# Performance work log

Measured on AMD Instinct MI355X. Metric: run time of the kernel, lower is better.

## Reference

```python
import jax, jax.numpy as jnp
import numpy as np

NUM_HEADS = 12
EPS = 1e-6

def setup_inputs() -> dict:
    key = jax.random.key(0)
    ks = jax.random.split(key, 7)
    B, N, C = 16, 4096, 384
    hd = C // NUM_HEADS
    s = 0.02
    return {
        "x": jax.random.normal(ks[0], (B, N, C), jnp.float32),
        "qkv_w": jax.random.normal(ks[1], (3 * C, C), jnp.float32) * s,
        "pos_enc": jax.random.normal(ks[2], (1, N, C), jnp.float32) * s,
        "dwc_w": jax.random.normal(ks[3], (hd, 1, 5, 5), jnp.float32) * s,
        "dwc_b": jnp.zeros((hd,), jnp.float32),
        "proj_w": jax.random.normal(ks[4], (C, C), jnp.float32) * s,
        "proj_b": jnp.zeros((C,), jnp.float32),
    }

def reference(x, qkv_w, pos_enc, dwc_w, dwc_b, proj_w, proj_b):
    B, N, C = x.shape
    H = NUM_HEADS
    hd = C // H
    qkv = x @ qkv_w.T  # (B, N, 3C)
    q, k, v = jnp.split(qkv, 3, axis=-1)
    k = k + pos_enc
    q = jax.nn.relu(q)
    k = jax.nn.relu(k)
    # b n (h c) -> (b h) n c
    def to_heads(t):
        return t.reshape(B, N, H, hd).transpose(0, 2, 1, 3).reshape(B * H, N, hd)
    q, k, v = to_heads(q), to_heads(k), to_heads(v)
    q = q.astype(jnp.float32); k = k.astype(jnp.float32); v = v.astype(jnp.float32)
    # normalizer z: (BH, N)
    z = 1.0 / (jnp.einsum('bic,bc->bi', q, k.sum(axis=1)) + EPS)
    # linear-attention branch (i*j*(c+d) > c*d*(i+j) here)
    kv = jnp.einsum('bjc,bjd->bcd', k, v)  # (BH, hd, hd)
    out = jnp.einsum('bic,bcd,bi->bid', q, kv, z)  # (BH, N, hd)
    # depthwise conv branch over v reshaped to spatial map
    w = int(np.sqrt(N))
    fm = v.reshape(B * H, w, w, hd).transpose(0, 3, 1, 2)  # b (w h) c -> b c w h
    fm = jax.lax.conv_general_dilated(
        fm, dwc_w, window_strides=(1, 1), padding=((2, 2), (2, 2)),
        feature_group_count=hd, dimension_numbers=('NCHW', 'OIHW', 'NCHW'))
    fm = fm + dwc_b[None, :, None, None]
    fm = fm.transpose(0, 2, 3, 1).reshape(B * H, N, hd)  # b c w h -> b (w h) c
    out = out + fm
    # (b h) n c -> b n (h c)
    out = out.reshape(B, H, N, hd).transpose(0, 2, 1, 3).reshape(B, N, C)
    return out @ proj_w.T + proj_b
```

## Files before the change

### kernel.cpp

```cpp
#include <hip/hip_runtime.h>
#include <hip/hip_bf16.h>
#include <cstdint>
#include <cstddef>


typedef __bf16 bf16;
typedef __attribute__((ext_vector_type(8))) __bf16 bf16x8;
typedef __attribute__((ext_vector_type(4))) __bf16 bf16x4;
typedef __attribute__((ext_vector_type(4))) float f32x4;
typedef __attribute__((ext_vector_type(16))) float f32x16;

#define NHEADS 12
#define HD 32
#define BATCH 16
#define SEQ 4096
#define CDIM 384
#define BHN (BATCH*NHEADS)
#define KVPARTS 2

__global__ void convert_w(const float* __restrict__ qkvw, const float* __restrict__ projw,
                          bf16* __restrict__ qkvw_b, bf16* __restrict__ projw_b) {
    int i = blockIdx.x * 256 + threadIdx.x;
    int stride = gridDim.x * 256;
    const int nq = 3 * CDIM * CDIM;
    const int np = CDIM * CDIM;
    for (int idx = i; idx < nq; idx += stride) qkvw_b[idx] = (bf16)qkvw[idx];
    for (int idx = i; idx < np; idx += stride) projw_b[idx] = (bf16)projw[idx];
}

__global__ __launch_bounds__(256, 2)
void gemm_qkv(const float* __restrict__ X, const bf16* __restrict__ Wb,
              const float* __restrict__ pos,
              bf16* __restrict__ qh, bf16* __restrict__ kh, bf16* __restrict__ vh) {
    __shared__ bf16 As[128 * 64];
    __shared__ bf16 Bs[128 * 64];
    const int tid  = threadIdx.x;
    const int lane = tid & 63;
    const int wid  = tid >> 6;
    const int m0   = blockIdx.y * 128;
    const int n0   = blockIdx.x * 128;
    const int wm   = (wid & 1) * 64;
    const int wn   = (wid >> 1) * 64;
    const int lr   = lane & 15;
    const int lq   = lane >> 4;

    f32x4 acc[4][4] = {};

    for (int k0 = 0; k0 < CDIM; k0 += 64) {
        #pragma unroll
        for (int it = 0; it < 4; ++it) {
            int cid = tid + it * 256;
            int r = cid >> 3, c = cid & 7;
            const float* srcA = X + (size_t)(m0 + r) * CDIM + k0 + c * 8;
            float4 f0 = *(const float4*)srcA;
            float4 f1 = *(const float4*)(srcA + 4);
            bf16x8 ha;
            ha[0]=(bf16)f0.x; ha[1]=(bf16)f0.y; ha[2]=(bf16)f0.z; ha[3]=(bf16)f0.w;
            ha[4]=(bf16)f1.x; ha[5]=(bf16)f1.y; ha[6]=(bf16)f1.z; ha[7]=(bf16)f1.w;
            *(bf16x8*)&As[r * 64 + ((c ^ (r & 7))) * 8] = ha;
            *(bf16x8*)&Bs[r * 64 + ((c ^ (r & 7))) * 8] =
                *(const bf16x8*)&Wb[(size_t)(n0 + r) * CDIM + k0 + c * 8];
        }
        __syncthreads();
        #pragma unroll
        for (int ks = 0; ks < 2; ++ks) {
            bf16x8 af[4], bfr[4];
            #pragma unroll
            for (int mi = 0; mi < 4; ++mi) {
                int r = wm + mi * 16 + lr;
                af[mi] = *(const bf16x8*)&As[r * 64 + ((ks * 4 + lq) ^ (r & 7)) * 8];
            }
            #pragma unroll
            for (int ni = 0; ni < 4; ++ni) {
                int r = wn + ni * 16 + lr;
                bfr[ni] = *(const bf16x8*)&Bs[r * 64 + ((ks * 4 + lq) ^ (r & 7)) * 8];
            }
            #pragma unroll
            for (int mi = 0; mi < 4; ++mi)
                #pragma unroll
                for (int ni = 0; ni < 4; ++ni)
                    acc[mi][ni] = __builtin_amdgcn_mfma_f32_16x16x32_bf16(
                        af[mi], bfr[ni], acc[mi][ni], 0, 0, 0);
        }
        __syncthreads();
    }

    const int sec = n0 / CDIM;
    #pragma unroll
    for (int mi = 0; mi < 4; ++mi) {
        #pragma unroll
        for (int ni = 0; ni < 4; ++ni) {
            int n = n0 + wn + ni * 16 + lr;
            int c = n - sec * CDIM;
            int hh = c >> 5, d = c & 31;
            #pragma unroll
            for (int r = 0; r < 4; ++r) {
                int m = m0 + wm + mi * 16 + lq * 4 + r;
                int b = m >> 12, i = m & 4095;
                float v = acc[mi][ni][r];
                size_t dst = ((size_t)(b * NHEADS + hh) * SEQ + i) * HD + d;
                if (sec == 0) {
                    qh[dst] = (bf16)fmaxf(v, 0.f);
                } else if (sec == 1) {
                    v += pos[(size_t)i * CDIM + c];
                    kh[dst] = (bf16)fmaxf(v, 0.f);
                } else {
                    vh[dst] = (bf16)v;
                }
            }
        }
    }
}

__global__ __launch_bounds__(256, 2)
void kv_mfma(const bf16* __restrict__ kh, const bf16* __restrict__ vh,
             float* __restrict__ kv_part, float* __restrict__ ksum_part) {
    __shared__ float red[4 * 1024];
    __shared__ float ksred[4 * 32];
    const int tid  = threadIdx.x;
    const int lane = tid & 63;
    const int w    = tid >> 6;
    const int bh   = blockIdx.y;
    const int part = blockIdx.x;
    const int col  = lane & 31;
    const int half = lane >> 5;
    const bf16* kb = kh + (size_t)bh * SEQ * HD;
    const bf16* vb = vh + (size_t)bh * SEQ * HD;
    const int j0 = part * 2048 + w * 512;

    f32x16 acc = {};
    f32x16 aks = {};
    bf16x8 ones;
    #pragma unroll
    for (int j = 0; j < 8; ++j) ones[j] = (bf16)1.0f;

    for (int s = 0; s < 32; ++s) {
        int jb = j0 + s * 16 + half * 8;
        bf16x8 afr, bfr;
        #pragma unroll
        for (int j = 0; j < 8; ++j) {
            afr[j] = kb[(size_t)(jb + j) * HD + col];
            bfr[j] = vb[(size_t)(jb + j) * HD + col];
        }
        acc = __builtin_amdgcn_mfma_f32_32x32x16_bf16(afr, bfr, acc, 0, 0, 0);
        aks = __builtin_amdgcn_mfma_f32_32x32x16_bf16(afr, ones, aks, 0, 0, 0);
    }

    #pragma unroll
    for (int r = 0; r < 16; ++r) {
        int row = (r & 3) + 8 * (r >> 2) + 4 * half;
        red[w * 1024 + row * 32 + col] = acc[r];
        ksred[w * 32 + row] = aks[r];
    }
    __syncthreads();
    {
        int e = tid * 4;
        f32x4 s4 = *(f32x4*)&red[e];
        s4 += *(f32x4*)&red[1024 + e];
        s4 += *(f32x4*)&red[2048 + e];
        s4 += *(f32x4*)&red[3072 + e];
        *(f32x4*)&kv_part[((size_t)bh * KVPARTS + part) * 1024 + e] = s4;
    }
    if (tid < 32) {
        ksum_part[((size_t)bh * KVPARTS + part) * 32 + tid] =
            ksred[tid] + ksred[32 + tid] + ksred[64 + tid] + ksred[96 + tid];
    }
}

__global__ __launch_bounds__(256, 2)
void attn_out(const bf16* __restrict__ qh, const bf16* __restrict__ vh,
              const float* __restrict__ kv_part, const float* __restrict__ ksum_part,
              const float* __restrict__ dwcw, const float* __restrict__ dwcb,
              bf16* __restrict__ outp) {
    __shared__ bf16 vt[12 * 64 * 32];
    __shared__ float kvl[1024];
    __shared__ float ksl[32];
    __shared__ float wl[25 * 32];
    __shared__ float bl[32];
    const int tid = threadIdx.x;
    const int bh  = blockIdx.y;
    const int ys  = blockIdx.x * 8;
    const bf16* vbase = vh + (size_t)bh * SEQ * HD;

    #pragma unroll
    for (int it = 0; it < 12; ++it) {
        int cid = tid + it * 256;
        int vy = cid >> 8;
        int xx = (cid >> 2) & 63;
        int q  = cid & 3;
        int gy = ys + vy - 2;
        bf16x8 val = {};
        if (gy >= 0 && gy < 64)
            val = *(const bf16x8*)&vbase[((size_t)gy * 64 + xx) * HD + q * 8];
        *(bf16x8*)&vt[(vy * 64 + xx) * HD + q * 8] = val;
    }
    {
        const float* kp = kv_part + (size_t)bh * KVPARTS * 1024;
        f32x4 t = *(const f32x4*)&kp[tid * 4];
        t += *(const f32x4*)&kp[1024 + tid * 4];
        *(f32x4*)&kvl[tid * 4] = t;
    }
    if (tid < 32) {
        const float* sp = ksum_part + (size_t)bh * KVPARTS * 32;
        ksl[tid] = sp[tid] + sp[32 + tid];
        #pragma unroll
        for (int tap = 0; tap < 25; ++tap) wl[tap * 32 + tid] = dwcw[tid * 25 + tap];
        bl[tid] = dwcb[tid];
    }
    __syncthreads();

    const int dq = tid & 7, d0 = dq * 4;
    const int ri = tid >> 3;
    const int b = bh / NHEADS, hh = bh % NHEADS;
    const bf16* qbase = qh + (size_t)bh * SEQ * HD;

    for (int it = 0; it < 16; ++it) {
        int pix = ri + it * 32;
        int yy = pix >> 6;
        int x  = pix & 63;
        int tok = (ys + yy) * 64 + x;
        float zden = 1e-6f;
        float dot0 = 0, dot1 = 0, dot2 = 0, dot3 = 0;
        #pragma unroll
        for (int c4 = 0; c4 < 32; c4 += 4) {
            bf16x4 qv = *(const bf16x4*)&qbase[(size_t)tok * HD + c4];
            #pragma unroll
            for (int u = 0; u < 4; ++u) {
                float qf = (float)qv[u];
                int c = c4 + u;
                zden += qf * ksl[c];
                dot0 += qf * kvl[c * 32 + d0];
                dot1 += qf * kvl[c * 32 + d0 + 1];
                dot2 += qf * kvl[c * 32 + d0 + 2];
                dot3 += qf * kvl[c * 32 + d0 + 3];
            }
        }
        float z = 1.f / zden;
        float f0 = bl[d0], f1 = bl[d0 + 1], f2 = bl[d0 + 2], f3 = bl[d0 + 3];
        int vyc = yy + 2;
        #pragma unroll
        for (int dy = -2; dy <= 2; ++dy) {
            #pragma unroll
            for (int dx = -2; dx <= 2; ++dx) {
                int xx = x + dx;
                if (xx < 0 || xx >= 64) continue;
                int tap = (dy + 2) * 5 + (dx + 2);
                bf16x4 vv = *(const bf16x4*)&vt[((vyc + dy) * 64 + xx) * HD + d0];
                const float* wp = &wl[tap * 32 + d0];
                f0 += (float)vv[0] * wp[0];
                f1 += (float)vv[1] * wp[1];
                f2 += (float)vv[2] * wp[2];
                f3 += (float)vv[3] * wp[3];
            }
        }
        bf16x4 ov;
        ov[0] = (bf16)(dot0 * z + f0);
        ov[1] = (bf16)(dot1 * z + f1);
        ov[2] = (bf16)(dot2 * z + f2);
        ov[3] = (bf16)(dot3 * z + f3);
        *(bf16x4*)&outp[((size_t)b * SEQ + tok) * CDIM + hh * HD + d0] = ov;
    }
}

__global__ __launch_bounds__(256, 2)
void gemm_proj(const bf16* __restrict__ A, const bf16* __restrict__ Wb,
               const float* __restrict__ bias, float* __restrict__ out) {
    __shared__ bf16 As[128 * 64];
    __shared__ bf16 Bs[128 * 64];
    const int tid  = threadIdx.x;
    const int lane = tid & 63;
    const int wid  = tid >> 6;
    const int m0   = blockIdx.y * 128;
    const int n0   = blockIdx.x * 128;
    const int wm   = (wid & 1) * 64;
    const int wn   = (wid >> 1) * 64;
    const int lr   = lane & 15;
    const int lq   = lane >> 4;

    f32x4 acc[4][4] = {};

    for (int k0 = 0; k0 < CDIM; k0 += 64) {
        #pragma unroll
        for (int it = 0; it < 4; ++it) {
            int cid = tid + it * 256;
            int r = cid >> 3, c = cid & 7;
            *(bf16x8*)&As[r * 64 + ((c ^ (r & 7))) * 8] =
                *(const bf16x8*)&A[(size_t)(m0 + r) * CDIM + k0 + c * 8];
            *(bf16x8*)&Bs[r * 64 + ((c ^ (r & 7))) * 8] =
                *(const bf16x8*)&Wb[(size_t)(n0 + r) * CDIM + k0 + c * 8];
        }
        __syncthreads();
        #pragma unroll
        for (int ks = 0; ks < 2; ++ks) {
            bf16x8 af[4], bfr[4];
            #pragma unroll
            for (int mi = 0; mi < 4; ++mi) {
                int r = wm + mi * 16 + lr;
                af[mi] = *(const bf16x8*)&As[r * 64 + ((ks * 4 + lq) ^ (r & 7)) * 8];
            }
            #pragma unroll
            for (int ni = 0; ni < 4; ++ni) {
                int r = wn + ni * 16 + lr;
                bfr[ni] = *(const bf16x8*)&Bs[r * 64 + ((ks * 4 + lq) ^ (r & 7)) * 8];
            }
            #pragma unroll
            for (int mi = 0; mi < 4; ++mi)
                #pragma unroll
                for (int ni = 0; ni < 4; ++ni)
                    acc[mi][ni] = __builtin_amdgcn_mfma_f32_16x16x32_bf16(
                        af[mi], bfr[ni], acc[mi][ni], 0, 0, 0);
        }
        __syncthreads();
    }

    #pragma unroll
    for (int mi = 0; mi < 4; ++mi) {
        #pragma unroll
        for (int ni = 0; ni < 4; ++ni) {
            int n = n0 + wn + ni * 16 + lr;
            float bv = bias[n];
            #pragma unroll
            for (int r = 0; r < 4; ++r) {
                int m = m0 + wm + mi * 16 + lq * 4 + r;
                out[(size_t)m * CDIM + n] = acc[mi][ni][r] + bv;
            }
        }
    }
}

extern "C" void kernel_launch(void* const* d_in, const int* in_sizes, int n_in,
                              void* d_out, int out_size, void* d_ws, size_t ws_size,
                              hipStream_t stream) {
    const float* x     = (const float*)d_in[0];
    const float* qkvw  = (const float*)d_in[1];
    const float* pos   = (const float*)d_in[2];
    const float* dwcw  = (const float*)d_in[3];
    const float* dwcb  = (const float*)d_in[4];
    const float* projw = (const float*)d_in[5];
    const float* projb = (const float*)d_in[6];
    float* out = (float*)d_out;

    char* ws = (char*)d_ws;
    size_t off = 0;
    auto alloc = [&](size_t bytes) -> void* {
        void* p = ws + off;
        off += (bytes + 255) & ~(size_t)255;
        return p;
    };
    bf16* qkvw_b = (bf16*)alloc((size_t)3 * CDIM * CDIM * 2);
    bf16* projw_b = (bf16*)alloc((size_t)CDIM * CDIM * 2);
    bf16* qh  = (bf16*)alloc((size_t)BHN * SEQ * HD * 2);
    bf16* khb = (bf16*)alloc((size_t)BHN * SEQ * HD * 2);
    bf16* vh  = (bf16*)alloc((size_t)BHN * SEQ * HD * 2);
    float* kvb   = (float*)alloc((size_t)BHN * KVPARTS * HD * HD * 4);
    float* ksumb = (float*)alloc((size_t)BHN * KVPARTS * HD * 4);

    hipLaunchKernelGGL(convert_w, dim3(512), dim3(256), 0, stream,
                       qkvw, projw, qkvw_b, projw_b);
    hipLaunchKernelGGL(gemm_qkv, dim3(9, 512), dim3(256), 0, stream,
                       x, qkvw_b, pos, qh, khb, vh);
    hipLaunchKernelGGL(kv_mfma, dim3(KVPARTS, BHN), dim3(256), 0, stream,
                       khb, vh, kvb, ksumb);
    bf16* outp = khb;
    hipLaunchKernelGGL(attn_out, dim3(8, BHN), dim3(256), 0, stream,
                       qh, vh, kvb, ksumb, dwcw, dwcb, outp);
    hipLaunchKernelGGL(gemm_proj, dim3(3, 512), dim3(256), 0, stream,
                       outp, projw_b, projb, out);
}
```

Before: 526.4 us.

## Pre-convert X to bf16 and use direct global-to-LDS loads in GEMMs

X is converted to bf16 in a separate vectorized pass, so gemm_qkv no longer converts fp32 tiles inline and re-reads fp32 X once for each of the nine N tiles. Both GEMMs now fill their LDS tiles with global_load_lds DMA, which skips the register round trip and keeps the XOR swizzle by permuting the source columns. Block indices are also remapped with an XCD-aware swizzle over a 1D grid so neighbouring tiles land on the same die's cache. The cost is an extra kernel pass that writes and re-reads a bf16 copy of X.

```diff
diff --git a/kernel.cpp b/kernel.cpp
--- a/kernel.cpp
+++ b/kernel.cpp
@@ -18,18 +18,52 @@
 #define BHN (BATCH*NHEADS)
 #define KVPARTS 2
 
-__global__ void convert_w(const float* __restrict__ qkvw, const float* __restrict__ projw,
-                          bf16* __restrict__ qkvw_b, bf16* __restrict__ projw_b) {
+__device__ __forceinline__ void gl_lds16(const bf16* g, bf16* l) {
+    __builtin_amdgcn_global_load_lds(
+        (const __attribute__((address_space(1))) unsigned int*)g,
+        (__attribute__((address_space(3))) unsigned int*)l, 16, 0, 0);
+}
+
+__global__ void convert_in(const float* __restrict__ X, const float* __restrict__ qkvw,
+                           const float* __restrict__ projw,
+                           bf16* __restrict__ xb, bf16* __restrict__ qkvw_b,
+                           bf16* __restrict__ projw_b) {
     int i = blockIdx.x * 256 + threadIdx.x;
     int stride = gridDim.x * 256;
-    const int nq = 3 * CDIM * CDIM;
-    const int np = CDIM * CDIM;
-    for (int idx = i; idx < nq; idx += stride) qkvw_b[idx] = (bf16)qkvw[idx];
-    for (int idx = i; idx < np; idx += stride) projw_b[idx] = (bf16)projw[idx];
+    const int nx = (65536 * CDIM) / 8;
+    for (int c = i; c < nx; c += stride) {
+        const float* s = X + (size_t)c * 8;
+        float4 f0 = *(const float4*)s;
+        float4 f1 = *(const float4*)(s + 4);
+        bf16x8 h;
+        h[0]=(bf16)f0.x; h[1]=(bf16)f0.y; h[2]=(bf16)f0.z; h[3]=(bf16)f0.w;
+        h[4]=(bf16)f1.x; h[5]=(bf16)f1.y; h[6]=(bf16)f1.z; h[7]=(bf16)f1.w;
+        *(bf16x8*)&xb[(size_t)c * 8] = h;
+    }
+    const int nq = (3 * CDIM * CDIM) / 8;
+    for (int c = i; c < nq; c += stride) {
+        const float* s = qkvw + (size_t)c * 8;
+        float4 f0 = *(const float4*)s;
+        float4 f1 = *(const float4*)(s + 4);
+        bf16x8 h;
+        h[0]=(bf16)f0.x; h[1]=(bf16)f0.y; h[2]=(bf16)f0.z; h[3]=(bf16)f0.w;
+        h[4]=(bf16)f1.x; h[5]=(bf16)f1.y; h[6]=(bf16)f1.z; h[7]=(bf16)f1.w;
+        *(bf16x8*)&qkvw_b[(size_t)c * 8] = h;
+    }
+    const int np = (CDIM * CDIM) / 8;
+    for (int c = i; c < np; c += stride) {
+        const float* s = projw + (size_t)c * 8;
+        float4 f0 = *(const float4*)s;
+        float4 f1 = *(const float4*)(s + 4);
+        bf16x8 h;
+        h[0]=(bf16)f0.x; h[1]=(bf16)f0.y; h[2]=(bf16)f0.z; h[3]=(bf16)f0.w;
+        h[4]=(bf16)f1.x; h[5]=(bf16)f1.y; h[6]=(bf16)f1.z; h[7]=(bf16)f1.w;
+        *(bf16x8*)&projw_b[(size_t)c * 8] = h;
+    }
 }
 
 __global__ __launch_bounds__(256, 2)
-void gemm_qkv(const float* __restrict__ X, const bf16* __restrict__ Wb,
+void gemm_qkv(const bf16* __restrict__ X, const bf16* __restrict__ Wb,
               const float* __restrict__ pos,
               bf16* __restrict__ qh, bf16* __restrict__ kh, bf16* __restrict__ vh) {
     __shared__ bf16 As[128 * 64];
@@ -37,29 +71,30 @@
     const int tid  = threadIdx.x;
     const int lane = tid & 63;
     const int wid  = tid >> 6;
-    const int m0   = blockIdx.y * 128;
-    const int n0   = blockIdx.x * 128;
+    const int blk  = blockIdx.x;
+    const int work = (blk & 7) * (4608 / 8) + (blk >> 3);
+    const int mt   = work / 9;
+    const int nt   = work - mt * 9;
+    const int m0   = mt * 128;
+    const int n0   = nt * 128;
     const int wm   = (wid & 1) * 64;
     const int wn   = (wid >> 1) * 64;
     const int lr   = lane & 15;
     const int lq   = lane >> 4;
 
+    const int srow = (lane >> 3);
+    const int sc   = lane & 7;
+
     f32x4 acc[4][4] = {};
 
     for (int k0 = 0; k0 < CDIM; k0 += 64) {
         #pragma unroll
         for (int it = 0; it < 4; ++it) {
-            int cid = tid + it * 256;
-            int r = cid >> 3, c = cid & 7;
-            const float* srcA = X + (size_t)(m0 + r) * CDIM + k0 + c * 8;
-            float4 f0 = *(const float4*)srcA;
-            float4 f1 = *(const float4*)(srcA + 4);
-            bf16x8 ha;
-            ha[0]=(bf16)f0.x; ha[1]=(bf16)f0.y; ha[2]=(bf16)f0.z; ha[3]=(bf16)f0.w;
-            ha[4]=(bf16)f1.x; ha[5]=(bf16)f1.y; ha[6]=(bf16)f1.z; ha[7]=(bf16)f1.w;
-            *(bf16x8*)&As[r * 64 + ((c ^ (r & 7))) * 8] = ha;
-            *(bf16x8*)&Bs[r * 64 + ((c ^ (r & 7))) * 8] =
-                *(const bf16x8*)&Wb[(size_t)(n0 + r) * CDIM + k0 + c * 8];
+            int rbase = wid * 32 + it * 8;
+            int r = rbase + srow;
+            int gc = sc ^ (r & 7);
+            gl_lds16(&X [(size_t)(m0 + r) * CDIM + k0 + gc * 8], &As[rbase * 64]);
+            gl_lds16(&Wb[(size_t)(n0 + r) * CDIM + k0 + gc * 8], &Bs[rbase * 64]);
         }
         __syncthreads();
         #pragma unroll
@@ -270,24 +305,29 @@
     const int tid  = threadIdx.x;
     const int lane = tid & 63;
     const int wid  = tid >> 6;
-    const int m0   = blockIdx.y * 128;
-    const int n0   = blockIdx.x * 128;
+    const int blk  = blockIdx.x;
+    const int work = (blk & 7) * (1536 / 8) + (blk >> 3);
+    const int mt   = work / 3;
+    const int nt   = work - mt * 3;
+    const int m0   = mt * 128;
+    const int n0   = nt * 128;
     const int wm   = (wid & 1) * 64;
     const int wn   = (wid >> 1) * 64;
     const int lr   = lane & 15;
     const int lq   = lane >> 4;
+    const int srow = (lane >> 3);
+    const int sc   = lane & 7;
 
     f32x4 acc[4][4] = {};
 
     for (int k0 = 0; k0 < CDIM; k0 += 64) {
         #pragma unroll
         for (int it = 0; it < 4; ++it) {
-            int cid = tid + it * 256;
-            int r = cid >> 3, c = cid & 7;
-            *(bf16x8*)&As[r * 64 + ((c ^ (r & 7))) * 8] =
-                *(const bf16x8*)&A[(size_t)(m0 + r) * CDIM + k0 + c * 8];
-            *(bf16x8*)&Bs[r * 64 + ((c ^ (r & 7))) * 8] =
-                *(const bf16x8*)&Wb[(size_t)(n0 + r) * CDIM + k0 + c * 8];
+            int rbase = wid * 32 + it * 8;
+            int r = rbase + srow;
+            int gc = sc ^ (r & 7);
+            gl_lds16(&A [(size_t)(m0 + r) * CDIM + k0 + gc * 8], &As[rbase * 64]);
+            gl_lds16(&Wb[(size_t)(n0 + r) * CDIM + k0 + gc * 8], &Bs[rbase * 64]);
         }
         __syncthreads();
         #pragma unroll
@@ -347,7 +387,8 @@
         off += (bytes + 255) & ~(size_t)255;
         return p;
     };
-    bf16* qkvw_b = (bf16*)alloc((size_t)3 * CDIM * CDIM * 2);
+    bf16* xb      = (bf16*)alloc((size_t)65536 * CDIM * 2);
+    bf16* qkvw_b  = (bf16*)alloc((size_t)3 * CDIM * CDIM * 2);
     bf16* projw_b = (bf16*)alloc((size_t)CDIM * CDIM * 2);
     bf16* qh  = (bf16*)alloc((size_t)BHN * SEQ * HD * 2);
     bf16* khb = (bf16*)alloc((size_t)BHN * SEQ * HD * 2);
@@ -355,15 +396,15 @@
     float* kvb   = (float*)alloc((size_t)BHN * KVPARTS * HD * HD * 4);
     float* ksumb = (float*)alloc((size_t)BHN * KVPARTS * HD * 4);
 
-    hipLaunchKernelGGL(convert_w, dim3(512), dim3(256), 0, stream,
-                       qkvw, projw, qkvw_b, projw_b);
-    hipLaunchKernelGGL(gemm_qkv, dim3(9, 512), dim3(256), 0, stream,
-                       x, qkvw_b, pos, qh, khb, vh);
+    hipLaunchKernelGGL(convert_in, dim3(2048), dim3(256), 0, stream,
+                       x, qkvw, projw, xb, qkvw_b, projw_b);
+    hipLaunchKernelGGL(gemm_qkv, dim3(4608), dim3(256), 0, stream,
+                       xb, qkvw_b, pos, qh, khb, vh);
     hipLaunchKernelGGL(kv_mfma, dim3(KVPARTS, BHN), dim3(256), 0, stream,
                        khb, vh, kvb, ksumb);
     bf16* outp = khb;
     hipLaunchKernelGGL(attn_out, dim3(8, BHN), dim3(256), 0, stream,
                        qh, vh, kvb, ksumb, dwcw, dwcb, outp);
-    hipLaunchKernelGGL(gemm_proj, dim3(3, 512), dim3(256), 0, stream,
+    hipLaunchKernelGGL(gemm_proj, dim3(1536), dim3(256), 0, stream,
                        outp, projw_b, projb, out);
 }
```

Result: faster. 475.6 us (-9.7%).
